# Kernel tuning notes

Measured on AMD Instinct MI355X. Metric: run time of the kernel, lower is better.

Reference implementation:

```python
import jax, jax.numpy as jnp
import numpy as np

C, T, H = 256, 16, 8
D = C // H  # head dim = 32
SCALE = float((D * T) ** 0.5)


def setup_inputs() -> dict:
    key = jax.random.key(0)
    kx, kk, kq, kv = jax.random.split(key, 4)
    B, P = 8, 1024
    x = jax.random.normal(kx, (B, C, P, T), dtype=jnp.float32)
    # 1x1 conv weights, no bias -> [out_ch, in_ch]
    Wk = jax.random.normal(kk, (C, C), dtype=jnp.float32) * 0.02
    Wq = jax.random.normal(kq, (C, C), dtype=jnp.float32) * 0.02
    Wv = jax.random.normal(kv, (C, C), dtype=jnp.float32) * 0.02
    return {"x": x, "Wk": Wk, "Wq": Wq, "Wv": Wv}


def _proj_split(W, x):
    # 1x1 conv == channel matmul, then split heads: b (h d) p t -> b h d p t
    B, _, P, Tt = x.shape
    y = jnp.einsum('oc,bcpt->bopt', W, x)
    return y.reshape(B, H, D, P, Tt)


def reference(x, Wk, Wq, Wv):
    B, _, P, Tt = x.shape
    k = _proj_split(Wk, x)  # [B,H,D,P,T]
    q = _proj_split(Wq, x)
    v = _proj_split(Wv, x)
    # energy over spatial positions, contracting head-dim and time
    energy = jnp.einsum('bhdpt,bhdqt->bhpq', k, q)  # [B,H,P,P]
    attn = jax.nn.softmax(energy / SCALE, axis=-1)
    out = jnp.einsum('bhpq,bhdpt->bhdqt', attn, v)  # [B,H,D,P,T]
    return out.reshape(B, C, P, Tt)
```

## Files before the change

### kernel.cpp

```cpp
#include <hip/hip_runtime.h>


typedef unsigned short u16;
typedef unsigned int u32;
typedef __attribute__((ext_vector_type(8))) short bfx8;
typedef __attribute__((ext_vector_type(4))) float fx4;

constexpr float KC1 = 1.4426950408889634f / 22.627416997969522f;

__device__ __forceinline__ u16 f2bf(float f) {
  u32 u = __builtin_bit_cast(u32, f);
  return (u16)((u + 0x7fffu + ((u >> 16) & 1u)) >> 16);
}
__device__ __forceinline__ float bf2f(u16 v) {
  return __builtin_bit_cast(float, (u32)v << 16);
}
__device__ __forceinline__ fx4 mfma16(bfx8 a, bfx8 b, fx4 c) {
  return __builtin_amdgcn_mfma_f32_16x16x32_bf16(a, b, c, 0, 0, 0);
}
typedef __attribute__((address_space(1))) const unsigned int* as1p;
typedef __attribute__((address_space(3))) unsigned int* as3p;
__device__ __forceinline__ void gll16(const void* g, void* l) {
  __builtin_amdgcn_global_load_lds((as1p)g, (as3p)l, 16, 0, 0);
}
__device__ __forceinline__ void midbar_() {
  __builtin_amdgcn_s_barrier();
}
__device__ __forceinline__ void pend_() {
  __builtin_amdgcn_s_barrier();
  __builtin_amdgcn_sched_barrier(0);
}
#define VMC4 do { asm volatile("s_waitcnt vmcnt(4)" ::: "memory"); \
                  __builtin_amdgcn_sched_barrier(0); } while (0)
#define VMC0 do { asm volatile("s_waitcnt vmcnt(0)" ::: "memory"); \
                  __builtin_amdgcn_sched_barrier(0); } while (0)

template <int NT, int LK>
__device__ __forceinline__ void gemm8(const u16* __restrict__ Ag,
                                      const u16* __restrict__ Bg,
                                      u16* lds, fx4 (&acc)[2][4][2][2],
                                      int wv, int lane) {
  const int l15 = lane & 15, kg = lane >> 4, l7 = lane & 7;
  const int wr = wv >> 2, wn = wv & 3;
  const int rsub = lane >> 3, csub = (lane & 7) * 8;
  constexpr int A0 = 0, A1 = 16384, B0 = 32768, B1 = 49152;
  bfx8 af[4][2], bf[2][2][2];

  auto stg = [&](const u16* g, int ldsoff, int tile, int half) {
    const u16* gp = g + (size_t)(half * 128 + wv * 16 + rsub) * LK + tile * 64 + csub;
    u16* lp = lds + ldsoff + half * 8192 + wv * 1024;
    gll16(gp, lp);
    gll16(gp + (size_t)8 * LK, lp + 512);
  };
  auto LA = [&](int boff, int mh) {
    const u16* base = lds + boff + mh * 8192 + wr * 4096;
#pragma unroll
    for (int mt = 0; mt < 4; ++mt)
#pragma unroll
      for (int kk = 0; kk < 2; ++kk)
        af[mt][kk] = *(const bfx8*)(base + (mt * 16 + l15) * 64 + (((kk << 2) + kg) ^ l7) * 8);
  };
  auto LB = [&](int boff, int nh) {
    const u16* base = lds + boff + nh * 8192 + wn * 2048;
#pragma unroll
    for (int nt = 0; nt < 2; ++nt)
#pragma unroll
      for (int kk = 0; kk < 2; ++kk)
        bf[nh][nt][kk] = *(const bfx8*)(base + (nt * 16 + l15) * 64 + (((kk << 2) + kg) ^ l7) * 8);
  };
  auto MM = [&](int mh, int nh) {
    __builtin_amdgcn_s_setprio(1);
#pragma unroll
    for (int mt = 0; mt < 4; ++mt)
#pragma unroll
      for (int nt = 0; nt < 2; ++nt)
#pragma unroll
        for (int kk = 0; kk < 2; ++kk)
          acc[mh][mt][nh][nt] = mfma16(af[mt][kk], bf[nh][nt][kk], acc[mh][mt][nh][nt]);
    __builtin_amdgcn_s_setprio(0);
  };

  stg(Ag, A0, 0, 0); stg(Ag, A0, 0, 1);
  stg(Bg, B0, 0, 0); stg(Bg, B0, 0, 1);
  stg(Ag, A1, 1, 0); stg(Bg, B1, 1, 1);
  VMC4;
  pend_();

  constexpr int NI = NT / 2;
#pragma unroll 1
  for (int i = 0; i < NI; ++i) {
    const int t = 2 * i;
    const bool more = (i + 1 < NI);
    LA(A0, 0); LB(B0, 0);
    stg(Ag, A1, t + 1, 1);
    midbar_();
    MM(0, 0);
    pend_();
    LB(B0, 1);
    stg(Bg, B1, t + 1, 0);
    midbar_();
    MM(0, 1);
    pend_();
    LA(A0, 1);
    if (more) stg(Ag, A0, t + 2, 0);
    midbar_();
    MM(1, 1);
    pend_();
    if (more) stg(Bg, B0, t + 2, 1);
    midbar_();
    MM(1, 0);
    if (more) { VMC4; } else { VMC0; }
    pend_();
    LA(A1, 0); LB(B1, 0);
    if (more) stg(Ag, A0, t + 2, 1);
    midbar_();
    MM(0, 0);
    pend_();
    LB(B1, 1);
    if (more) stg(Bg, B0, t + 2, 0);
    midbar_();
    MM(0, 1);
    pend_();
    LA(A1, 1);
    if (more) stg(Ag, A1, t + 3, 0);
    midbar_();
    MM(1, 1);
    pend_();
    if (more) stg(Bg, B1, t + 3, 1);
    midbar_();
    MM(1, 0);
    if (more) { VMC4; }
    pend_();
  }
}

__global__ __launch_bounds__(256) void k_wconv(const float* __restrict__ Wk,
                                               const float* __restrict__ Wq,
                                               const float* __restrict__ Wv,
                                               u16* __restrict__ Wall) {
  int blk = blockIdx.x;
  int pr = blk >> 5;
  const float* src = (pr == 0) ? Wk : ((pr == 1) ? Wq : Wv);
  int oc = (blk & 31) * 8 + (threadIdx.x >> 5);
  int Cc = threadIdx.x & 31;
  const float4* s4 = (const float4*)(src + oc * 256 + Cc * 8);
  float4 a = s4[0], b = s4[1];
  alignas(16) u16 t[8] = {f2bf(a.x), f2bf(a.y), f2bf(a.z), f2bf(a.w),
                          f2bf(b.x), f2bf(b.y), f2bf(b.z), f2bf(b.w)};
  int o = pr * 256 + oc;
  int pos = (Cc & ~7) + ((Cc & 7) ^ (o & 7));
  *(uint4*)(Wall + o * 256 + pos * 8) = *(const uint4*)t;
}

__global__ __launch_bounds__(256) void k_xt(const float* __restrict__ x,
                                            u16* __restrict__ Xbf) {
  __shared__ u16 Xs[128 * 256];
  int b = blockIdx.x >> 7;
  int n0 = (blockIdx.x & 127) * 128;
  int tid = threadIdx.x;
  int ng = tid & 31, cgrp = tid >> 5;
  const float* xb = x + (size_t)b * 4194304 + n0 + ng * 4;
#pragma unroll
  for (int it = 0; it < 4; ++it) {
    int Cc = cgrp + it * 8;
    float4 v[8];
#pragma unroll
    for (int i = 0; i < 8; ++i)
      v[i] = *(const float4*)(xb + (size_t)(Cc * 8 + i) * 16384);
#pragma unroll
    for (int j = 0; j < 4; ++j) {
      int n = ng * 4 + j;
      alignas(16) u16 c8[8];
#pragma unroll
      for (int i = 0; i < 8; ++i) c8[i] = f2bf(((const float*)&v[i])[j]);
      int pos = (Cc & ~7) + ((Cc & 7) ^ (n & 7));
      *(uint4*)&Xs[n * 256 + pos * 8] = *(const uint4*)c8;
    }
  }
  __syncthreads();
  u16* xo = Xbf + (size_t)b * 4194304 + (size_t)n0 * 256;
#pragma unroll
  for (int it = 0; it < 16; ++it) {
    int idx = tid + it * 256;
    int n = idx >> 5, chp = idx & 31;
    uint4 v = *(const uint4*)&Xs[n * 256 + chp * 8];
    *(uint4*)&xo[(size_t)n * 256 + chp * 8] = v;
  }
}

__global__ __launch_bounds__(512) void k_proj2(const u16* __restrict__ Xbf,
                                               const u16* __restrict__ Wall,
                                               u16* __restrict__ Kb, u16* __restrict__ Qb,
                                               u16* __restrict__ Vb) {
  __shared__ u16 lds[65536];
  int bid = blockIdx.x;
  int vid = (bid & 7) * 192 + (bid >> 3);
  int nidx = vid / 3;
  int otile = vid - nidx * 3;
  int b = nidx >> 6, ntile = nidx & 63;
  int tid = threadIdx.x, lane = tid & 63, wv = tid >> 6;
  int l15 = lane & 15, kg = lane >> 4;
  int wr = wv >> 2, wn = wv & 3;
  const u16* Ag = Wall + otile * 65536;
  const u16* Bg = Xbf + (size_t)b * 4194304 + (size_t)ntile * 65536;
  fx4 acc[2][4][2][2];
#pragma unroll
  for (int mh = 0; mh < 2; ++mh)
#pragma unroll
    for (int mt = 0; mt < 4; ++mt)
#pragma unroll
      for (int nh = 0; nh < 2; ++nh)
#pragma unroll
        for (int nt = 0; nt < 2; ++nt) acc[mh][mt][nh][nt] = (fx4)0.0f;

  gemm8<4, 256>(Ag, Bg, lds, acc, wv, lane);

  u16* dst = (otile == 0) ? Kb : ((otile == 1) ? Qb : Vb);
#pragma unroll
  for (int mh = 0; mh < 2; ++mh)
#pragma unroll
    for (int mt = 0; mt < 4; ++mt) {
      int o = mh * 128 + wr * 64 + mt * 16 + kg * 4;
      int h = o >> 5;
      size_t bhro = (size_t)(b * 8 + h) * 524288;
#pragma unroll
      for (int nh = 0; nh < 2; ++nh)
#pragma unroll
        for (int nt = 0; nt < 2; ++nt) {
          int p = ntile * 16 + nh * 8 + wn * 2 + nt;
          size_t ro = bhro + (size_t)p * 512;
          int p7 = p & 7;
#pragma unroll
          for (int j = 0; j < 4; ++j) {
            int f = ((o & 31) + j) * 16 + l15;
            int ch = (f >> 3) ^ p7;
            dst[ro + ch * 8 + (f & 7)] = f2bf(acc[mh][mt][nh][nt][j]);
          }
        }
    }
}

__global__ __launch_bounds__(512) void k_egemm(const u16* __restrict__ Qb,
                                               const u16* __restrict__ Kb,
                                               u16* __restrict__ Pt,
                                               float* __restrict__ Zpart) {
  __shared__ u16 lds[65536];
  int bid = blockIdx.x;
  int vid = (bid & 7) * 128 + (bid >> 3);
  int bh = vid >> 4, tile = vid & 15;
  int q0 = (tile >> 2) * 256, p0 = (tile & 3) * 256;
  int tid = threadIdx.x, lane = tid & 63, wv = tid >> 6;
  int l15 = lane & 15, kg = lane >> 4;
  int wr = wv >> 2, wn = wv & 3;
  const u16* Ag = Qb + (size_t)bh * 524288 + (size_t)q0 * 512;
  const u16* Bg = Kb + (size_t)bh * 524288 + (size_t)p0 * 512;
  fx4 acc[2][4][2][2];
#pragma unroll
  for (int mh = 0; mh < 2; ++mh)
#pragma unroll
    for (int mt = 0; mt < 4; ++mt)
#pragma unroll
      for (int nh = 0; nh < 2; ++nh)
#pragma unroll
        for (int nt = 0; nt < 2; ++nt) acc[mh][mt][nh][nt] = (fx4)0.0f;

  gemm8<8, 512>(Ag, Bg, lds, acc, wv, lane);

  float zl[2][2] = {{0.f, 0.f}, {0.f, 0.f}};
  size_t pbase = (size_t)bh * 1048576;
#pragma unroll
  for (int mh = 0; mh < 2; ++mh)
#pragma unroll
    for (int mt = 0; mt < 4; ++mt) {
      int qb_ = q0 + mh * 128 + wr * 64 + mt * 16 + kg * 4;
#pragma unroll
      for (int nh = 0; nh < 2; ++nh)
#pragma unroll
        for (int nt = 0; nt < 2; ++nt) {
          int p = p0 + nh * 128 + wn * 32 + nt * 16 + l15;
#pragma unroll
          for (int j = 0; j < 4; ++j) {
            int q = qb_ + j;
            float e = exp2f(acc[mh][mt][nh][nt][j] * KC1);
            zl[nh][nt] += e;
            Pt[pbase + (size_t)q * 1024 + (((p >> 3) ^ (q & 7)) * 8 + (p & 7))] = f2bf(e);
          }
        }
    }
  float* Zl = (float*)lds;
#pragma unroll
  for (int nh = 0; nh < 2; ++nh)
#pragma unroll
    for (int nt = 0; nt < 2; ++nt) {
      float v = zl[nh][nt];
      v += __shfl_xor(v, 16);
      v += __shfl_xor(v, 32);
      zl[nh][nt] = v;
    }
  __syncthreads();
  if (lane < 16) {
#pragma unroll
    for (int nh = 0; nh < 2; ++nh)
#pragma unroll
      for (int nt = 0; nt < 2; ++nt)
        Zl[wr * 256 + nh * 128 + wn * 32 + nt * 16 + lane] = zl[nh][nt];
  }
  __syncthreads();
  if (tid < 256) {
    float s = Zl[tid] + Zl[256 + tid];
    Zpart[(size_t)(tile >> 2) * 65536 + (size_t)bh * 1024 + p0 + tid] = s;
  }
}

__global__ __launch_bounds__(256) void k_zfinal(const float* __restrict__ Zpart,
                                                float* __restrict__ RZ) {
  int idx = blockIdx.x * 256 + threadIdx.x;
  float s = Zpart[idx] + Zpart[65536 + idx] + Zpart[131072 + idx] + Zpart[196608 + idx];
  RZ[idx] = 1.0f / s;
}

__global__ __launch_bounds__(256) void k_vt(const u16* __restrict__ Vb,
                                            const float* __restrict__ RZ,
                                            u16* __restrict__ Vt) {
  __shared__ u16 Vl[64 * 512];
  int bh = blockIdx.x >> 4;
  int ptile = blockIdx.x & 15;
  int tid = threadIdx.x;
  const u16* src = Vb + (size_t)bh * 524288 + (size_t)ptile * 32768;
#pragma unroll
  for (int it = 0; it < 16; ++it) {
    int idx = tid + it * 256;
    int pl = idx >> 6, g = idx & 63;
    float rz = RZ[bh * 1024 + ptile * 64 + pl];
    uint4 v = *(const uint4*)&src[(size_t)pl * 512 + g * 8];
    int cf = g ^ (pl & 7);
    u32 w[4] = {v.x, v.y, v.z, v.w};
    alignas(16) u16 c8[8];
#pragma unroll
    for (int i = 0; i < 4; ++i) {
      c8[2 * i]     = f2bf(bf2f((u16)w[i]) * rz);
      c8[2 * i + 1] = f2bf(bf2f((u16)(w[i] >> 16)) * rz);
    }
    *(uint4*)&Vl[pl * 512 + cf * 8] = *(const uint4*)c8;
  }
  __syncthreads();
  u16* dst = Vt + (size_t)bh * 524288;
#pragma unroll
  for (int it = 0; it < 16; ++it) {
    int f = (tid & 63) + (it & 7) * 64;
    int pc = (tid >> 6) * 2 + (it >> 3);
    int base = pc * 8 * 512 + f;
    u32 x0 = (u32)Vl[base] | ((u32)Vl[base + 512] << 16);
    u32 x1 = (u32)Vl[base + 1024] | ((u32)Vl[base + 1536] << 16);
    u32 x2 = (u32)Vl[base + 2048] | ((u32)Vl[base + 2560] << 16);
    u32 x3 = (u32)Vl[base + 3072] | ((u32)Vl[base + 3584] << 16);
    uint4 pk; pk.x = x0; pk.y = x1; pk.z = x2; pk.w = x3;
    int col = ptile * 8 + (pc ^ (f & 7));
    *(uint4*)&dst[(size_t)f * 1024 + col * 8] = pk;
  }
}

__global__ __launch_bounds__(512) void k_pv(const u16* __restrict__ Pt,
                                            const u16* __restrict__ Vt,
                                            float* __restrict__ out) {
  __shared__ u16 lds[65536];
  int bid = blockIdx.x;
  int vid = (bid & 7) * 64 + (bid >> 3);
  int bh = vid >> 3, tile = vid & 7;
  int q0 = (tile >> 1) * 256, f0 = (tile & 1) * 256;
  int tid = threadIdx.x, lane = tid & 63, wv = tid >> 6;
  int l15 = lane & 15, kg = lane >> 4;
  int wr = wv >> 2, wn = wv & 3;
  const u16* Ag = Pt + (size_t)bh * 1048576 + (size_t)q0 * 1024;
  const u16* Bg = Vt + (size_t)bh * 524288 + (size_t)f0 * 1024;
  fx4 acc[2][4][2][2];
#pragma unroll
  for (int mh = 0; mh < 2; ++mh)
#pragma unroll
    for (int mt = 0; mt < 4; ++mt)
#pragma unroll
      for (int nh = 0; nh < 2; ++nh)
#pragma unroll
        for (int nt = 0; nt < 2; ++nt) acc[mh][mt][nh][nt] = (fx4)0.0f;

  gemm8<16, 1024>(Ag, Bg, lds, acc, wv, lane);

#pragma unroll
  for (int mh = 0; mh < 2; ++mh)
#pragma unroll
    for (int mt = 0; mt < 4; ++mt) {
      int qb_ = q0 + mh * 128 + wr * 64 + mt * 16 + kg * 4;
#pragma unroll
      for (int nh = 0; nh < 2; ++nh)
#pragma unroll
        for (int nt = 0; nt < 2; ++nt) {
          int f = f0 + nh * 128 + wn * 32 + nt * 16 + l15;
          int d = f >> 4, t = f & 15;
          size_t cb = (size_t)(bh * 32 + d) * 16384 + t;
#pragma unroll
          for (int j = 0; j < 4; ++j) out[cb + (size_t)(qb_ + j) * 16] = acc[mh][mt][nh][nt][j];
        }
    }
}

extern "C" void kernel_launch(void* const* d_in, const int* in_sizes, int n_in,
                              void* d_out, int out_size, void* d_ws, size_t ws_size,
                              hipStream_t stream) {
  (void)in_sizes; (void)n_in; (void)out_size; (void)ws_size;
  const float* x  = (const float*)d_in[0];
  const float* Wk = (const float*)d_in[1];
  const float* Wq = (const float*)d_in[2];
  const float* Wv = (const float*)d_in[3];
  float* out = (float*)d_out;

  u16* Kb  = (u16*)d_ws;
  u16* Qb  = Kb + 33554432;
  u16* Vb  = Qb + 33554432;
  u16* Xbf = Vb + 33554432;
  u16* Pt  = Xbf;
  u16* Vt  = Qb;
  float* Zpart = (float*)(Kb + 167772160);
  float* RZ = Zpart + 262144;
  u16* Wall = (u16*)(RZ + 65536);

  k_wconv<<<96, 256, 0, stream>>>(Wk, Wq, Wv, Wall);
  k_xt<<<1024, 256, 0, stream>>>(x, Xbf);
  k_proj2<<<1536, 512, 0, stream>>>(Xbf, Wall, Kb, Qb, Vb);
  k_egemm<<<1024, 512, 0, stream>>>(Qb, Kb, Pt, Zpart);
  k_zfinal<<<256, 256, 0, stream>>>(Zpart, RZ);
  k_vt<<<1024, 256, 0, stream>>>(Vb, RZ, Vt);
  k_pv<<<512, 512, 0, stream>>>(Pt, Vt, out);
}
```

Baseline: 351.5 us.

## Make GEMM blocks persistent over several output tiles with streaming epilogues

The shared GEMM helper gains a multi-segment mode: each workgroup keeps its A tile fixed and loops over several B (or A) tiles, calling an epilogue lambda after every segment and then resetting its accumulators. proj2 computes K, Q and V in one block, and egemm and pv each sweep all column tiles for a fixed q-tile, so the grids become 512, 256 and 256 blocks. The aim is to reuse staged inputs and overlap prefetch of the next segment with the epilogue stores. egemm now writes its partial row sums per warp row (Zpart doubles in size) and uses swapped MFMA operands to get 8-byte Pt stores. The smaller grids lower occupancy and parallelism, and a VMC0 drain follows each epilogue.

Result: slower. 442.7 us (+26.0%).

```diff
diff --git a/kernel.cpp b/kernel.cpp
--- a/kernel.cpp
+++ b/kernel.cpp
@@ -23,9 +23,7 @@
 __device__ __forceinline__ void gll16(const void* g, void* l) {
   __builtin_amdgcn_global_load_lds((as1p)g, (as3p)l, 16, 0, 0);
 }
-__device__ __forceinline__ void midbar_() {
-  __builtin_amdgcn_s_barrier();
-}
+__device__ __forceinline__ void midbar_() { __builtin_amdgcn_s_barrier(); }
 __device__ __forceinline__ void pend_() {
   __builtin_amdgcn_s_barrier();
   __builtin_amdgcn_sched_barrier(0);
@@ -35,19 +33,21 @@
 #define VMC0 do { asm volatile("s_waitcnt vmcnt(0)" ::: "memory"); \
                   __builtin_amdgcn_sched_barrier(0); } while (0)
 
-template <int NT, int LK>
-__device__ __forceinline__ void gemm8(const u16* __restrict__ Ag,
-                                      const u16* __restrict__ Bg,
-                                      u16* lds, fx4 (&acc)[2][4][2][2],
-                                      int wv, int lane) {
+template <bool SWAP, int NT, int SL, int LK, int ASTR, int BSTR, typename Epi>
+__device__ __forceinline__ void gemm8m(const u16* __restrict__ Ag,
+                                       const u16* __restrict__ Bg,
+                                       u16* lds, fx4 (&acc)[2][4][2][2],
+                                       int wv, int lane, Epi&& epi) {
   const int l15 = lane & 15, kg = lane >> 4, l7 = lane & 7;
   const int wr = wv >> 2, wn = wv & 3;
   const int rsub = lane >> 3, csub = (lane & 7) * 8;
   constexpr int A0 = 0, A1 = 16384, B0 = 32768, B1 = 49152;
+  constexpr int TM = (1 << SL) - 1;
   bfx8 af[4][2], bf[2][2][2];
 
-  auto stg = [&](const u16* g, int ldsoff, int tile, int half) {
-    const u16* gp = g + (size_t)(half * 128 + wv * 16 + rsub) * LK + tile * 64 + csub;
+  auto stg = [&](const u16* g, int sstr, int ldsoff, int t, int half) {
+    const u16* gp = g + (size_t)(t >> SL) * (size_t)sstr + (t & TM) * 64
+                  + (size_t)(half * 128 + wv * 16 + rsub) * LK + csub;
     u16* lp = lds + ldsoff + half * 8192 + wv * 1024;
     gll16(gp, lp);
     gll16(gp + (size_t)8 * LK, lp + 512);
@@ -75,62 +75,55 @@
 #pragma unroll
       for (int nt = 0; nt < 2; ++nt)
 #pragma unroll
-        for (int kk = 0; kk < 2; ++kk)
-          acc[mh][mt][nh][nt] = mfma16(af[mt][kk], bf[nh][nt][kk], acc[mh][mt][nh][nt]);
+        for (int kk = 0; kk < 2; ++kk) {
+          if constexpr (SWAP)
+            acc[mh][mt][nh][nt] = mfma16(bf[nh][nt][kk], af[mt][kk], acc[mh][mt][nh][nt]);
+          else
+            acc[mh][mt][nh][nt] = mfma16(af[mt][kk], bf[nh][nt][kk], acc[mh][mt][nh][nt]);
+        }
     __builtin_amdgcn_s_setprio(0);
   };
 
-  stg(Ag, A0, 0, 0); stg(Ag, A0, 0, 1);
-  stg(Bg, B0, 0, 0); stg(Bg, B0, 0, 1);
-  stg(Ag, A1, 1, 0); stg(Bg, B1, 1, 1);
+  stg(Ag, ASTR, A0, 0, 0); stg(Ag, ASTR, A0, 0, 1);
+  stg(Bg, BSTR, B0, 0, 0); stg(Bg, BSTR, B0, 0, 1);
+  stg(Ag, ASTR, A1, 1, 0); stg(Bg, BSTR, B1, 1, 1);
   VMC4;
   pend_();
 
-  constexpr int NI = NT / 2;
 #pragma unroll 1
-  for (int i = 0; i < NI; ++i) {
+  for (int i = 0; i < NT / 2; ++i) {
     const int t = 2 * i;
-    const bool more = (i + 1 < NI);
+    const bool m2 = (t + 2 < NT), m3 = (t + 3 < NT);
     LA(A0, 0); LB(B0, 0);
-    stg(Ag, A1, t + 1, 1);
-    midbar_();
-    MM(0, 0);
-    pend_();
+    stg(Ag, ASTR, A1, t + 1, 1);
+    midbar_(); MM(0, 0); pend_();
     LB(B0, 1);
-    stg(Bg, B1, t + 1, 0);
-    midbar_();
-    MM(0, 1);
-    pend_();
+    stg(Bg, BSTR, B1, t + 1, 0);
+    midbar_(); MM(0, 1); pend_();
     LA(A0, 1);
-    if (more) stg(Ag, A0, t + 2, 0);
-    midbar_();
-    MM(1, 1);
-    pend_();
-    if (more) stg(Bg, B0, t + 2, 1);
-    midbar_();
-    MM(1, 0);
-    if (more) { VMC4; } else { VMC0; }
+    if (m2) stg(Ag, ASTR, A0, t + 2, 0);
+    midbar_(); MM(1, 1); pend_();
+    if (m2) stg(Bg, BSTR, B0, t + 2, 1);
+    midbar_(); MM(1, 0);
+    if (m2) { VMC4; } else { VMC0; }
     pend_();
     LA(A1, 0); LB(B1, 0);
-    if (more) stg(Ag, A0, t + 2, 1);
-    midbar_();
-    MM(0, 0);
+    if (m2) stg(Ag, ASTR, A0, t + 2, 1);
+    midbar_(); MM(0, 0); pend_();
+    LB(B1, 1);
+    if (m2) stg(Bg, BSTR, B0, t + 2, 0);
+    midbar_(); MM(0, 1); pend_();
+    LA(A1, 1);
+    if (m3) stg(Ag, ASTR, A1, t + 3, 0);
+    midbar_(); MM(1, 1); pend_();
+    if (m3) stg(Bg, BSTR, B1, t + 3, 1);
+    midbar_(); MM(1, 0);
+    if (m2) { VMC4; }
     pend_();
-    LB(B1, 1);
-    if (more) stg(Bg, B0, t + 2, 0);
-    midbar_();
-    MM(0, 1);
-    pend_();
-    LA(A1, 1);
-    if (more) stg(Ag, A1, t + 3, 0);
-    midbar_();
-    MM(1, 1);
-    pend_();
-    if (more) stg(Bg, B1, t + 3, 1);
-    midbar_();
-    MM(1, 0);
-    if (more) { VMC4; }
-    pend_();
+    if (((t + 2) & TM) == 0) {
+      epi((t + 1) >> SL);
+      if (t + 2 < NT) { VMC0; }
+    }
   }
 }
 
@@ -194,14 +187,12 @@
                                                u16* __restrict__ Vb) {
   __shared__ u16 lds[65536];
   int bid = blockIdx.x;
-  int vid = (bid & 7) * 192 + (bid >> 3);
-  int nidx = vid / 3;
-  int otile = vid - nidx * 3;
-  int b = nidx >> 6, ntile = nidx & 63;
+  int vid = (bid & 7) * 64 + (bid >> 3);
+  int b = vid >> 6, ntile = vid & 63;
   int tid = threadIdx.x, lane = tid & 63, wv = tid >> 6;
   int l15 = lane & 15, kg = lane >> 4;
   int wr = wv >> 2, wn = wv & 3;
-  const u16* Ag = Wall + otile * 65536;
+  const u16* Ag = Wall;
   const u16* Bg = Xbf + (size_t)b * 4194304 + (size_t)ntile * 65536;
   fx4 acc[2][4][2][2];
 #pragma unroll
@@ -213,31 +204,34 @@
 #pragma unroll
         for (int nt = 0; nt < 2; ++nt) acc[mh][mt][nh][nt] = (fx4)0.0f;
 
-  gemm8<4, 256>(Ag, Bg, lds, acc, wv, lane);
-
-  u16* dst = (otile == 0) ? Kb : ((otile == 1) ? Qb : Vb);
-#pragma unroll
-  for (int mh = 0; mh < 2; ++mh)
-#pragma unroll
-    for (int mt = 0; mt < 4; ++mt) {
-      int o = mh * 128 + wr * 64 + mt * 16 + kg * 4;
-      int h = o >> 5;
-      size_t bhro = (size_t)(b * 8 + h) * 524288;
-#pragma unroll
-      for (int nh = 0; nh < 2; ++nh)
-#pragma unroll
-        for (int nt = 0; nt < 2; ++nt) {
-          int p = ntile * 16 + nh * 8 + wn * 2 + nt;
-          size_t ro = bhro + (size_t)p * 512;
-          int p7 = p & 7;
-#pragma unroll
-          for (int j = 0; j < 4; ++j) {
-            int f = ((o & 31) + j) * 16 + l15;
-            int ch = (f >> 3) ^ p7;
-            dst[ro + ch * 8 + (f & 7)] = f2bf(acc[mh][mt][nh][nt][j]);
+  auto epi = [&](int s) {
+    u16* dst = (s == 0) ? Kb : ((s == 1) ? Qb : Vb);
+#pragma unroll
+    for (int mh = 0; mh < 2; ++mh)
+#pragma unroll
+      for (int mt = 0; mt < 4; ++mt) {
+        int o = mh * 128 + wr * 64 + mt * 16 + kg * 4;
+        int h = o >> 5;
+        size_t bhro = (size_t)(b * 8 + h) * 524288;
+#pragma unroll
+        for (int nh = 0; nh < 2; ++nh)
+#pragma unroll
+          for (int nt = 0; nt < 2; ++nt) {
+            int p = ntile * 16 + nh * 8 + wn * 2 + nt;
+            size_t ro = bhro + (size_t)p * 512;
+            int p7 = p & 7;
+#pragma unroll
+            for (int j = 0; j < 4; ++j) {
+              int f = ((o & 31) + j) * 16 + l15;
+              int ch = (f >> 3) ^ p7;
+              dst[ro + ch * 8 + (f & 7)] = f2bf(acc[mh][mt][nh][nt][j]);
+            }
+            acc[mh][mt][nh][nt] = (fx4)0.0f;
           }
-        }
-    }
+      }
+  };
+
+  gemm8m<false, 12, 2, 256, 65536, 0>(Ag, Bg, lds, acc, wv, lane, epi);
 }
 
 __global__ __launch_bounds__(512) void k_egemm(const u16* __restrict__ Qb,
@@ -246,14 +240,15 @@
                                                float* __restrict__ Zpart) {
   __shared__ u16 lds[65536];
   int bid = blockIdx.x;
-  int vid = (bid & 7) * 128 + (bid >> 3);
-  int bh = vid >> 4, tile = vid & 15;
-  int q0 = (tile >> 2) * 256, p0 = (tile & 3) * 256;
+  int vid = (bid & 7) * 32 + (bid >> 3);
+  int bh = vid >> 2, qt = vid & 3;
+  int q0 = qt * 256;
   int tid = threadIdx.x, lane = tid & 63, wv = tid >> 6;
   int l15 = lane & 15, kg = lane >> 4;
   int wr = wv >> 2, wn = wv & 3;
   const u16* Ag = Qb + (size_t)bh * 524288 + (size_t)q0 * 512;
-  const u16* Bg = Kb + (size_t)bh * 524288 + (size_t)p0 * 512;
+  const u16* Bg = Kb + (size_t)bh * 524288;
+  size_t pbase = (size_t)bh * 1048576;
   fx4 acc[2][4][2][2];
 #pragma unroll
   for (int mh = 0; mh < 2; ++mh)
@@ -264,58 +259,76 @@
 #pragma unroll
         for (int nt = 0; nt < 2; ++nt) acc[mh][mt][nh][nt] = (fx4)0.0f;
 
-  gemm8<8, 512>(Ag, Bg, lds, acc, wv, lane);
-
-  float zl[2][2] = {{0.f, 0.f}, {0.f, 0.f}};
-  size_t pbase = (size_t)bh * 1048576;
-#pragma unroll
-  for (int mh = 0; mh < 2; ++mh)
-#pragma unroll
-    for (int mt = 0; mt < 4; ++mt) {
-      int qb_ = q0 + mh * 128 + wr * 64 + mt * 16 + kg * 4;
+  auto epi = [&](int s) {
+    float zac[2][2][4];
+#pragma unroll
+    for (int nh = 0; nh < 2; ++nh)
+#pragma unroll
+      for (int nt = 0; nt < 2; ++nt)
+#pragma unroll
+        for (int j = 0; j < 4; ++j) zac[nh][nt][j] = 0.f;
+#pragma unroll
+    for (int mh = 0; mh < 2; ++mh)
+#pragma unroll
+      for (int mt = 0; mt < 4; ++mt) {
+        int q = q0 + mh * 128 + wr * 64 + mt * 16 + l15;
+        size_t qrow = pbase + (size_t)q * 1024;
+        int q7 = l15 & 7;
+#pragma unroll
+        for (int nh = 0; nh < 2; ++nh)
+#pragma unroll
+          for (int nt = 0; nt < 2; ++nt) {
+            int p4 = s * 256 + nh * 128 + wn * 32 + nt * 16 + kg * 4;
+            alignas(8) u16 e4[4];
+#pragma unroll
+            for (int j = 0; j < 4; ++j) {
+              float e = exp2f(acc[mh][mt][nh][nt][j] * KC1);
+              zac[nh][nt][j] += e;
+              e4[j] = f2bf(e);
+            }
+            int ch = (p4 >> 3) ^ q7;
+            *(unsigned long long*)(Pt + qrow + ch * 8 + (p4 & 7)) =
+                *(const unsigned long long*)e4;
+            acc[mh][mt][nh][nt] = (fx4)0.0f;
+          }
+      }
+#pragma unroll
+    for (int nh = 0; nh < 2; ++nh)
+#pragma unroll
+      for (int nt = 0; nt < 2; ++nt)
+#pragma unroll
+        for (int j = 0; j < 4; ++j) {
+          float v = zac[nh][nt][j];
+          v += __shfl_xor(v, 1);
+          v += __shfl_xor(v, 2);
+          v += __shfl_xor(v, 4);
+          v += __shfl_xor(v, 8);
+          zac[nh][nt][j] = v;
+        }
+    if (l15 == 0) {
+      size_t zb = (size_t)(qt * 2 + wr) * 65536 + (size_t)bh * 1024;
 #pragma unroll
       for (int nh = 0; nh < 2; ++nh)
 #pragma unroll
         for (int nt = 0; nt < 2; ++nt) {
-          int p = p0 + nh * 128 + wn * 32 + nt * 16 + l15;
-#pragma unroll
-          for (int j = 0; j < 4; ++j) {
-            int q = qb_ + j;
-            float e = exp2f(acc[mh][mt][nh][nt][j] * KC1);
-            zl[nh][nt] += e;
-            Pt[pbase + (size_t)q * 1024 + (((p >> 3) ^ (q & 7)) * 8 + (p & 7))] = f2bf(e);
-          }
+          int p4 = s * 256 + nh * 128 + wn * 32 + nt * 16 + kg * 4;
+          float4 zv;
+          zv.x = zac[nh][nt][0]; zv.y = zac[nh][nt][1];
+          zv.z = zac[nh][nt][2]; zv.w = zac[nh][nt][3];
+          *(float4*)&Zpart[zb + p4] = zv;
         }
     }
-  float* Zl = (float*)lds;
-#pragma unroll
-  for (int nh = 0; nh < 2; ++nh)
-#pragma unroll
-    for (int nt = 0; nt < 2; ++nt) {
-      float v = zl[nh][nt];
-      v += __shfl_xor(v, 16);
-      v += __shfl_xor(v, 32);
-      zl[nh][nt] = v;
-    }
-  __syncthreads();
-  if (lane < 16) {
-#pragma unroll
-    for (int nh = 0; nh < 2; ++nh)
-#pragma unroll
-      for (int nt = 0; nt < 2; ++nt)
-        Zl[wr * 256 + nh * 128 + wn * 32 + nt * 16 + lane] = zl[nh][nt];
-  }
-  __syncthreads();
-  if (tid < 256) {
-    float s = Zl[tid] + Zl[256 + tid];
-    Zpart[(size_t)(tile >> 2) * 65536 + (size_t)bh * 1024 + p0 + tid] = s;
-  }
+  };
+
+  gemm8m<true, 32, 3, 512, 0, 131072>(Ag, Bg, lds, acc, wv, lane, epi);
 }
 
 __global__ __launch_bounds__(256) void k_zfinal(const float* __restrict__ Zpart,
                                                 float* __restrict__ RZ) {
   int idx = blockIdx.x * 256 + threadIdx.x;
-  float s = Zpart[idx] + Zpart[65536 + idx] + Zpart[131072 + idx] + Zpart[196608 + idx];
+  float s = 0.f;
+#pragma unroll
+  for (int k = 0; k < 8; ++k) s += Zpart[(size_t)k * 65536 + idx];
   RZ[idx] = 1.0f / s;
 }
 
@@ -365,14 +378,14 @@
                                             float* __restrict__ out) {
   __shared__ u16 lds[65536];
   int bid = blockIdx.x;
-  int vid = (bid & 7) * 64 + (bid >> 3);
-  int bh = vid >> 3, tile = vid & 7;
-  int q0 = (tile >> 1) * 256, f0 = (tile & 1) * 256;
+  int vid = (bid & 7) * 32 + (bid >> 3);
+  int bh = vid >> 2, qt = vid & 3;
+  int q0 = qt * 256;
   int tid = threadIdx.x, lane = tid & 63, wv = tid >> 6;
   int l15 = lane & 15, kg = lane >> 4;
   int wr = wv >> 2, wn = wv & 3;
   const u16* Ag = Pt + (size_t)bh * 1048576 + (size_t)q0 * 1024;
-  const u16* Bg = Vt + (size_t)bh * 524288 + (size_t)f0 * 1024;
+  const u16* Bg = Vt + (size_t)bh * 524288;
   fx4 acc[2][4][2][2];
 #pragma unroll
   for (int mh = 0; mh < 2; ++mh)
@@ -383,24 +396,28 @@
 #pragma unroll
         for (int nt = 0; nt < 2; ++nt) acc[mh][mt][nh][nt] = (fx4)0.0f;
 
-  gemm8<16, 1024>(Ag, Bg, lds, acc, wv, lane);
-
-#pragma unroll
-  for (int mh = 0; mh < 2; ++mh)
-#pragma unroll
-    for (int mt = 0; mt < 4; ++mt) {
-      int qb_ = q0 + mh * 128 + wr * 64 + mt * 16 + kg * 4;
-#pragma unroll
-      for (int nh = 0; nh < 2; ++nh)
-#pragma unroll
-        for (int nt = 0; nt < 2; ++nt) {
-          int f = f0 + nh * 128 + wn * 32 + nt * 16 + l15;
-          int d = f >> 4, t = f & 15;
-          size_t cb = (size_t)(bh * 32 + d) * 16384 + t;
-#pragma unroll
-          for (int j = 0; j < 4; ++j) out[cb + (size_t)(qb_ + j) * 16] = acc[mh][mt][nh][nt][j];
-        }
-    }
+  auto epi = [&](int s) {
+#pragma unroll
+    for (int mh = 0; mh < 2; ++mh)
+#pragma unroll
+      for (int mt = 0; mt < 4; ++mt) {
+        int qb_ = q0 + mh * 128 + wr * 64 + mt * 16 + kg * 4;
+#pragma unroll
+        for (int nh = 0; nh < 2; ++nh)
+#pragma unroll
+          for (int nt = 0; nt < 2; ++nt) {
+            int f = s * 256 + nh * 128 + wn * 32 + nt * 16 + l15;
+            int d = f >> 4, t = f & 15;
+            size_t cb = (size_t)(bh * 32 + d) * 16384 + t;
+#pragma unroll
+            for (int j = 0; j < 4; ++j)
+              out[cb + (size_t)(qb_ + j) * 16] = acc[mh][mt][nh][nt][j];
+            acc[mh][mt][nh][nt] = (fx4)0.0f;
+          }
+      }
+  };
+
+  gemm8m<false, 32, 4, 1024, 0, 262144>(Ag, Bg, lds, acc, wv, lane, epi);
 }
 
 extern "C" void kernel_launch(void* const* d_in, const int* in_sizes, int n_in,
@@ -420,14 +437,14 @@
   u16* Pt  = Xbf;
   u16* Vt  = Qb;
   float* Zpart = (float*)(Kb + 167772160);
-  float* RZ = Zpart + 262144;
+  float* RZ = Zpart + 524288;
   u16* Wall = (u16*)(RZ + 65536);
 
   k_wconv<<<96, 256, 0, stream>>>(Wk, Wq, Wv, Wall);
   k_xt<<<1024, 256, 0, stream>>>(x, Xbf);
-  k_proj2<<<1536, 512, 0, stream>>>(Xbf, Wall, Kb, Qb, Vb);
-  k_egemm<<<1024, 512, 0, stream>>>(Qb, Kb, Pt, Zpart);
+  k_proj2<<<512, 512, 0, stream>>>(Xbf, Wall, Kb, Qb, Vb);
+  k_egemm<<<256, 512, 0, stream>>>(Qb, Kb, Pt, Zpart);
   k_zfinal<<<256, 256, 0, stream>>>(Zpart, RZ);
   k_vt<<<1024, 256, 0, stream>>>(Vb, RZ, Vt);
-  k_pv<<<512, 512, 0, stream>>>(Pt, Vt, out);
-}
+  k_pv<<<256, 512, 0, stream>>>(Pt, Vt, out);
+}
```

## Use 256x128 register-prefetch GEMM tiles for energy and PV kernels

Applied to the files above, without the earlier changes.

Adds a new GEMM core (gemm_rp) that uses 256x128 tiles with 2x4 waves, a 4x4 accumulator per wave, double-buffered LDS, and register prefetch of fragments across k-steps. The energy and PV kernels now use it, which doubles their grid sizes and cuts LDS to 96KB so more blocks can be resident. The energy kernel uses a swapped MFMA operand order so each lane writes 4 contiguous P values as 64-bit stores, and it reduces row sums with shuffles into 16 partial slices instead of going through LDS. The trade-off is less reuse per tile, more partial-sum traffic in k_zfinal, and a VMC0 full wait on every k-step in place of the earlier partial vmcnt pipelining.

Measured after the change: 431.0 us. 22.6% more time.

```diff
diff --git a/kernel.cpp b/kernel.cpp
--- a/kernel.cpp
+++ b/kernel.cpp
@@ -3,6 +3,7 @@
 
 typedef unsigned short u16;
 typedef unsigned int u32;
+typedef unsigned long long u64;
 typedef __attribute__((ext_vector_type(8))) short bfx8;
 typedef __attribute__((ext_vector_type(4))) float fx4;
 
@@ -23,17 +24,105 @@
 __device__ __forceinline__ void gll16(const void* g, void* l) {
   __builtin_amdgcn_global_load_lds((as1p)g, (as3p)l, 16, 0, 0);
 }
-__device__ __forceinline__ void midbar_() {
-  __builtin_amdgcn_s_barrier();
-}
+__device__ __forceinline__ void midbar_() { __builtin_amdgcn_s_barrier(); }
 __device__ __forceinline__ void pend_() {
   __builtin_amdgcn_s_barrier();
   __builtin_amdgcn_sched_barrier(0);
 }
-#define VMC4 do { asm volatile("s_waitcnt vmcnt(4)" ::: "memory"); \
-                  __builtin_amdgcn_sched_barrier(0); } while (0)
-#define VMC0 do { asm volatile("s_waitcnt vmcnt(0)" ::: "memory"); \
-                  __builtin_amdgcn_sched_barrier(0); } while (0)
+#define SB0 __builtin_amdgcn_sched_barrier(0)
+#define VMC4 do { asm volatile("s_waitcnt vmcnt(4)" ::: "memory"); SB0; } while (0)
+#define VMC0 do { asm volatile("s_waitcnt vmcnt(0)" ::: "memory"); SB0; } while (0)
+
+template <bool SWAP, int NT, int LK>
+__device__ __forceinline__ void gemm_rp(const u16* __restrict__ Ag,
+                                        const u16* __restrict__ Bg,
+                                        u16* lds, fx4 (&acc)[4][4],
+                                        int wv, int lane) {
+  const int l15 = lane & 15, kg = lane >> 4, l7 = lane & 7;
+  const int wr = wv >> 1, wc = wv & 1;
+  const int rs8 = lane >> 3, c8 = (lane & 7) * 8;
+  constexpr int AS0 = 0, AS1 = 16384, BS0 = 32768, BS1 = 40960;
+  bfx8 af[4][2], bf[4][2];
+
+  auto stgA = [&](int t, int aoff) {
+#pragma unroll
+    for (int i = 0; i < 4; ++i)
+      gll16(Ag + (size_t)(wv * 32 + i * 8 + rs8) * LK + t * 64 + c8,
+            lds + aoff + (wv * 32 + i * 8) * 64);
+  };
+  auto stgB = [&](int t, int boff) {
+#pragma unroll
+    for (int i = 0; i < 2; ++i)
+      gll16(Bg + (size_t)(wv * 16 + i * 8 + rs8) * LK + t * 64 + c8,
+            lds + boff + (wv * 16 + i * 8) * 64);
+  };
+  auto RA = [&](int kk, int aoff) {
+#pragma unroll
+    for (int mt = 0; mt < 4; ++mt)
+      af[mt][kk] = *(const bfx8*)(lds + aoff + (wr * 64 + mt * 16 + l15) * 64 +
+                                  (((kk << 2) + kg) ^ l7) * 8);
+  };
+  auto RB = [&](int kk, int ng, int boff) {
+#pragma unroll
+    for (int q = 0; q < 2; ++q) {
+      int nt = ng * 2 + q;
+      bf[nt][kk] = *(const bfx8*)(lds + boff + (wc * 64 + nt * 16 + l15) * 64 +
+                                  (((kk << 2) + kg) ^ l7) * 8);
+    }
+  };
+  auto MM = [&](int kk, int ng) {
+    __builtin_amdgcn_s_setprio(1);
+#pragma unroll
+    for (int mt = 0; mt < 4; ++mt)
+#pragma unroll
+      for (int q = 0; q < 2; ++q) {
+        int nt = ng * 2 + q;
+        if constexpr (SWAP)
+          acc[mt][nt] = mfma16(bf[nt][kk], af[mt][kk], acc[mt][nt]);
+        else
+          acc[mt][nt] = mfma16(af[mt][kk], bf[nt][kk], acc[mt][nt]);
+      }
+    __builtin_amdgcn_s_setprio(0);
+  };
+
+  stgA(0, AS0); stgB(0, BS0);
+  VMC0;
+  __builtin_amdgcn_s_barrier();
+  SB0;
+  RA(0, AS0); RB(0, 0, BS0);
+
+#pragma unroll 1
+  for (int t = 0; t < NT - 1; ++t) {
+    const int cA = (t & 1) ? AS1 : AS0, nA = (t & 1) ? AS0 : AS1;
+    const int cB = (t & 1) ? BS1 : BS0, nB = (t & 1) ? BS0 : BS1;
+    stgA(t + 1, nA); stgB(t + 1, nB);
+    RB(0, 1, cB);
+    MM(0, 0);
+    SB0;
+    RA(1, cA); RB(1, 0, cB);
+    MM(0, 1);
+    SB0;
+    RB(1, 1, cB);
+    MM(1, 0);
+    VMC0;
+    __builtin_amdgcn_s_barrier();
+    SB0;
+    RA(0, nA); RB(0, 0, nB);
+    MM(1, 1);
+    SB0;
+  }
+  {
+    constexpr int cAo = ((NT - 1) & 1) ? AS1 : AS0;
+    constexpr int cBo = ((NT - 1) & 1) ? BS1 : BS0;
+    RB(0, 1, cBo);
+    MM(0, 0); SB0;
+    RA(1, cAo); RB(1, 0, cBo);
+    MM(0, 1); SB0;
+    RB(1, 1, cBo);
+    MM(1, 0); SB0;
+    MM(1, 1); SB0;
+  }
+}
 
 template <int NT, int LK>
 __device__ __forceinline__ void gemm8(const u16* __restrict__ Ag,
@@ -93,42 +182,28 @@
     const bool more = (i + 1 < NI);
     LA(A0, 0); LB(B0, 0);
     stg(Ag, A1, t + 1, 1);
-    midbar_();
-    MM(0, 0);
-    pend_();
+    midbar_(); MM(0, 0); pend_();
     LB(B0, 1);
     stg(Bg, B1, t + 1, 0);
-    midbar_();
-    MM(0, 1);
-    pend_();
+    midbar_(); MM(0, 1); pend_();
     LA(A0, 1);
     if (more) stg(Ag, A0, t + 2, 0);
-    midbar_();
-    MM(1, 1);
-    pend_();
+    midbar_(); MM(1, 1); pend_();
     if (more) stg(Bg, B0, t + 2, 1);
-    midbar_();
-    MM(1, 0);
+    midbar_(); MM(1, 0);
     if (more) { VMC4; } else { VMC0; }
     pend_();
     LA(A1, 0); LB(B1, 0);
     if (more) stg(Ag, A0, t + 2, 1);
-    midbar_();
-    MM(0, 0);
-    pend_();
+    midbar_(); MM(0, 0); pend_();
     LB(B1, 1);
     if (more) stg(Bg, B0, t + 2, 0);
-    midbar_();
-    MM(0, 1);
-    pend_();
+    midbar_(); MM(0, 1); pend_();
     LA(A1, 1);
     if (more) stg(Ag, A1, t + 3, 0);
-    midbar_();
-    MM(1, 1);
-    pend_();
+    midbar_(); MM(1, 1); pend_();
     if (more) stg(Bg, B1, t + 3, 1);
-    midbar_();
-    MM(1, 0);
+    midbar_(); MM(1, 0);
     if (more) { VMC4; }
     pend_();
   }
@@ -170,11 +245,11 @@
 #pragma unroll
     for (int j = 0; j < 4; ++j) {
       int n = ng * 4 + j;
-      alignas(16) u16 c8[8];
-#pragma unroll
-      for (int i = 0; i < 8; ++i) c8[i] = f2bf(((const float*)&v[i])[j]);
+      alignas(16) u16 c8v[8];
+#pragma unroll
+      for (int i = 0; i < 8; ++i) c8v[i] = f2bf(((const float*)&v[i])[j]);
       int pos = (Cc & ~7) + ((Cc & 7) ^ (n & 7));
-      *(uint4*)&Xs[n * 256 + pos * 8] = *(const uint4*)c8;
+      *(uint4*)&Xs[n * 256 + pos * 8] = *(const uint4*)c8v;
     }
   }
   __syncthreads();
@@ -244,78 +319,78 @@
                                                const u16* __restrict__ Kb,
                                                u16* __restrict__ Pt,
                                                float* __restrict__ Zpart) {
-  __shared__ u16 lds[65536];
+  __shared__ u16 lds[49152];
   int bid = blockIdx.x;
-  int vid = (bid & 7) * 128 + (bid >> 3);
-  int bh = vid >> 4, tile = vid & 15;
-  int q0 = (tile >> 2) * 256, p0 = (tile & 3) * 256;
+  int vid = (bid & 7) * 256 + (bid >> 3);
+  int bh = vid >> 5, qt = (vid >> 3) & 3, pt = vid & 7;
+  int q0 = qt * 256, p0 = pt * 128;
   int tid = threadIdx.x, lane = tid & 63, wv = tid >> 6;
-  int l15 = lane & 15, kg = lane >> 4;
-  int wr = wv >> 2, wn = wv & 3;
+  int l15 = lane & 15, kg = lane >> 4, l7 = lane & 7;
+  int wr = wv >> 1, wc = wv & 1;
   const u16* Ag = Qb + (size_t)bh * 524288 + (size_t)q0 * 512;
   const u16* Bg = Kb + (size_t)bh * 524288 + (size_t)p0 * 512;
-  fx4 acc[2][4][2][2];
-#pragma unroll
-  for (int mh = 0; mh < 2; ++mh)
-#pragma unroll
-    for (int mt = 0; mt < 4; ++mt)
-#pragma unroll
-      for (int nh = 0; nh < 2; ++nh)
-#pragma unroll
-        for (int nt = 0; nt < 2; ++nt) acc[mh][mt][nh][nt] = (fx4)0.0f;
-
-  gemm8<8, 512>(Ag, Bg, lds, acc, wv, lane);
-
-  float zl[2][2] = {{0.f, 0.f}, {0.f, 0.f}};
+  fx4 acc[4][4];
+#pragma unroll
+  for (int mt = 0; mt < 4; ++mt)
+#pragma unroll
+    for (int nt = 0; nt < 4; ++nt) acc[mt][nt] = (fx4)0.0f;
+
+  gemm_rp<true, 8, 512>(Ag, Bg, lds, acc, wv, lane);
+
   size_t pbase = (size_t)bh * 1048576;
-#pragma unroll
-  for (int mh = 0; mh < 2; ++mh)
-#pragma unroll
-    for (int mt = 0; mt < 4; ++mt) {
-      int qb_ = q0 + mh * 128 + wr * 64 + mt * 16 + kg * 4;
-#pragma unroll
-      for (int nh = 0; nh < 2; ++nh)
-#pragma unroll
-        for (int nt = 0; nt < 2; ++nt) {
-          int p = p0 + nh * 128 + wn * 32 + nt * 16 + l15;
-#pragma unroll
-          for (int j = 0; j < 4; ++j) {
-            int q = qb_ + j;
-            float e = exp2f(acc[mh][mt][nh][nt][j] * KC1);
-            zl[nh][nt] += e;
-            Pt[pbase + (size_t)q * 1024 + (((p >> 3) ^ (q & 7)) * 8 + (p & 7))] = f2bf(e);
-          }
-        }
-    }
-  float* Zl = (float*)lds;
-#pragma unroll
-  for (int nh = 0; nh < 2; ++nh)
-#pragma unroll
-    for (int nt = 0; nt < 2; ++nt) {
-      float v = zl[nh][nt];
-      v += __shfl_xor(v, 16);
-      v += __shfl_xor(v, 32);
-      zl[nh][nt] = v;
-    }
-  __syncthreads();
-  if (lane < 16) {
-#pragma unroll
-    for (int nh = 0; nh < 2; ++nh)
-#pragma unroll
-      for (int nt = 0; nt < 2; ++nt)
-        Zl[wr * 256 + nh * 128 + wn * 32 + nt * 16 + lane] = zl[nh][nt];
-  }
-  __syncthreads();
-  if (tid < 256) {
-    float s = Zl[tid] + Zl[256 + tid];
-    Zpart[(size_t)(tile >> 2) * 65536 + (size_t)bh * 1024 + p0 + tid] = s;
+  float zac[4][4];
+#pragma unroll
+  for (int nt = 0; nt < 4; ++nt)
+#pragma unroll
+    for (int j = 0; j < 4; ++j) zac[nt][j] = 0.f;
+#pragma unroll
+  for (int mt = 0; mt < 4; ++mt) {
+    int q = q0 + wr * 64 + mt * 16 + l15;
+    size_t qrow = pbase + (size_t)q * 1024;
+#pragma unroll
+    for (int nt = 0; nt < 4; ++nt) {
+      int p4 = p0 + wc * 64 + nt * 16 + kg * 4;
+      alignas(8) u16 e4[4];
+#pragma unroll
+      for (int j = 0; j < 4; ++j) {
+        float e = exp2f(acc[mt][nt][j] * KC1);
+        zac[nt][j] += e;
+        e4[j] = f2bf(e);
+      }
+      int ch = (p4 >> 3) ^ l7;
+      *(u64*)(Pt + qrow + ch * 8 + (p4 & 7)) = *(const u64*)e4;
+    }
+  }
+#pragma unroll
+  for (int nt = 0; nt < 4; ++nt)
+#pragma unroll
+    for (int j = 0; j < 4; ++j) {
+      float v = zac[nt][j];
+      v += __shfl_xor(v, 1);
+      v += __shfl_xor(v, 2);
+      v += __shfl_xor(v, 4);
+      v += __shfl_xor(v, 8);
+      zac[nt][j] = v;
+    }
+  if (l15 == 0) {
+    size_t zb = (size_t)(qt * 4 + wr) * 65536 + (size_t)bh * 1024;
+#pragma unroll
+    for (int nt = 0; nt < 4; ++nt) {
+      int p4 = p0 + wc * 64 + nt * 16 + kg * 4;
+      float4 zv;
+      zv.x = zac[nt][0]; zv.y = zac[nt][1];
+      zv.z = zac[nt][2]; zv.w = zac[nt][3];
+      *(float4*)&Zpart[zb + p4] = zv;
+    }
   }
 }
 
 __global__ __launch_bounds__(256) void k_zfinal(const float* __restrict__ Zpart,
                                                 float* __restrict__ RZ) {
   int idx = blockIdx.x * 256 + threadIdx.x;
-  float s = Zpart[idx] + Zpart[65536 + idx] + Zpart[131072 + idx] + Zpart[196608 + idx];
+  float s = 0.f;
+#pragma unroll
+  for (int k = 0; k < 16; ++k) s += Zpart[(size_t)k * 65536 + idx];
   RZ[idx] = 1.0f / s;
 }
 
@@ -335,13 +410,13 @@
     uint4 v = *(const uint4*)&src[(size_t)pl * 512 + g * 8];
     int cf = g ^ (pl & 7);
     u32 w[4] = {v.x, v.y, v.z, v.w};
-    alignas(16) u16 c8[8];
+    alignas(16) u16 c8v[8];
 #pragma unroll
     for (int i = 0; i < 4; ++i) {
-      c8[2 * i]     = f2bf(bf2f((u16)w[i]) * rz);
-      c8[2 * i + 1] = f2bf(bf2f((u16)(w[i] >> 16)) * rz);
-    }
-    *(uint4*)&Vl[pl * 512 + cf * 8] = *(const uint4*)c8;
+      c8v[2 * i]     = f2bf(bf2f((u16)w[i]) * rz);
+      c8v[2 * i + 1] = f2bf(bf2f((u16)(w[i] >> 16)) * rz);
+    }
+    *(uint4*)&Vl[pl * 512 + cf * 8] = *(const uint4*)c8v;
   }
   __syncthreads();
   u16* dst = Vt + (size_t)bh * 524288;
@@ -363,44 +438,37 @@
 __global__ __launch_bounds__(512) void k_pv(const u16* __restrict__ Pt,
                                             const u16* __restrict__ Vt,
                                             float* __restrict__ out) {
-  __shared__ u16 lds[65536];
+  __shared__ u16 lds[49152];
   int bid = blockIdx.x;
-  int vid = (bid & 7) * 64 + (bid >> 3);
-  int bh = vid >> 3, tile = vid & 7;
-  int q0 = (tile >> 1) * 256, f0 = (tile & 1) * 256;
+  int vid = (bid & 7) * 128 + (bid >> 3);
+  int bh = vid >> 4, qt = (vid >> 2) & 3, ft = vid & 3;
+  int q0 = qt * 256, f0 = ft * 128;
   int tid = threadIdx.x, lane = tid & 63, wv = tid >> 6;
   int l15 = lane & 15, kg = lane >> 4;
-  int wr = wv >> 2, wn = wv & 3;
+  int wr = wv >> 1, wc = wv & 1;
   const u16* Ag = Pt + (size_t)bh * 1048576 + (size_t)q0 * 1024;
   const u16* Bg = Vt + (size_t)bh * 524288 + (size_t)f0 * 1024;
-  fx4 acc[2][4][2][2];
-#pragma unroll
-  for (int mh = 0; mh < 2; ++mh)
-#pragma unroll
-    for (int mt = 0; mt < 4; ++mt)
-#pragma unroll
-      for (int nh = 0; nh < 2; ++nh)
-#pragma unroll
-        for (int nt = 0; nt < 2; ++nt) acc[mh][mt][nh][nt] = (fx4)0.0f;
-
-  gemm8<16, 1024>(Ag, Bg, lds, acc, wv, lane);
-
-#pragma unroll
-  for (int mh = 0; mh < 2; ++mh)
-#pragma unroll
-    for (int mt = 0; mt < 4; ++mt) {
-      int qb_ = q0 + mh * 128 + wr * 64 + mt * 16 + kg * 4;
-#pragma unroll
-      for (int nh = 0; nh < 2; ++nh)
-#pragma unroll
-        for (int nt = 0; nt < 2; ++nt) {
-          int f = f0 + nh * 128 + wn * 32 + nt * 16 + l15;
-          int d = f >> 4, t = f & 15;
-          size_t cb = (size_t)(bh * 32 + d) * 16384 + t;
-#pragma unroll
-          for (int j = 0; j < 4; ++j) out[cb + (size_t)(qb_ + j) * 16] = acc[mh][mt][nh][nt][j];
-        }
-    }
+  fx4 acc[4][4];
+#pragma unroll
+  for (int mt = 0; mt < 4; ++mt)
+#pragma unroll
+    for (int nt = 0; nt < 4; ++nt) acc[mt][nt] = (fx4)0.0f;
+
+  gemm_rp<false, 16, 1024>(Ag, Bg, lds, acc, wv, lane);
+
+#pragma unroll
+  for (int mt = 0; mt < 4; ++mt) {
+    int qb_ = q0 + wr * 64 + mt * 16 + kg * 4;
+#pragma unroll
+    for (int nt = 0; nt < 4; ++nt) {
+      int f = f0 + wc * 64 + nt * 16 + l15;
+      int d = f >> 4, t = f & 15;
+      size_t cb = (size_t)(bh * 32 + d) * 16384 + t;
+#pragma unroll
+      for (int j = 0; j < 4; ++j)
+        out[cb + (size_t)(qb_ + j) * 16] = acc[mt][nt][j];
+    }
+  }
 }
 
 extern "C" void kernel_launch(void* const* d_in, const int* in_sizes, int n_in,
@@ -420,14 +488,14 @@
   u16* Pt  = Xbf;
   u16* Vt  = Qb;
   float* Zpart = (float*)(Kb + 167772160);
-  float* RZ = Zpart + 262144;
+  float* RZ = Zpart + 1048576;
   u16* Wall = (u16*)(RZ + 65536);
 
   k_wconv<<<96, 256, 0, stream>>>(Wk, Wq, Wv, Wall);
   k_xt<<<1024, 256, 0, stream>>>(x, Xbf);
   k_proj2<<<1536, 512, 0, stream>>>(Xbf, Wall, Kb, Qb, Vb);
-  k_egemm<<<1024, 512, 0, stream>>>(Qb, Kb, Pt, Zpart);
+  k_egemm<<<2048, 512, 0, stream>>>(Qb, Kb, Pt, Zpart);
   k_zfinal<<<256, 256, 0, stream>>>(Zpart, RZ);
   k_vt<<<1024, 256, 0, stream>>>(Vb, RZ, Vt);
-  k_pv<<<512, 512, 0, stream>>>(Pt, Vt, out);
-}
+  k_pv<<<1024, 512, 0, stream>>>(Pt, Vt, out);
+}
```
